# Kernel optimization log

Hardware: AMD Instinct MI355X
Metric: run time of the kernel (lower is better)

The kernel has to match this reference:

```python
import jax, jax.numpy as jnp
import numpy as np

EPS = 1e-7
CURVS = (1.0, 0.8, 1.2)
SCALES = (1.0, 0.8, 0.6)


def expmap0(v, c):
    sc = jnp.sqrt(c)
    n = jnp.maximum(jnp.linalg.norm(v, axis=-1, keepdims=True), EPS)
    return jnp.tanh(sc * n) * v / (sc * n)


def projx(x, c):
    max_n = (1.0 - 1e-5) / jnp.sqrt(c)
    n = jnp.maximum(jnp.linalg.norm(x, axis=-1, keepdims=True), EPS)
    return jnp.where(n > max_n, x * (max_n / n), x)


def logmap0(x, c):
    sc = jnp.sqrt(c)
    n = jnp.maximum(jnp.linalg.norm(x, axis=-1, keepdims=True), EPS)
    a = jnp.clip(sc * n, 0.0, 1.0 - 1e-7)
    return jnp.arctanh(a) * x / (sc * n)


def hamilton(q1, q2):
    # q1, q2: [..., 4] (w,x,y,z), broadcasting allowed
    w1, x1, y1, z1 = q1[..., 0], q1[..., 1], q1[..., 2], q1[..., 3]
    w2, x2, y2, z2 = q2[..., 0], q2[..., 1], q2[..., 2], q2[..., 3]
    w = w1 * w2 - x1 * x2 - y1 * y2 - z1 * z2
    x = w1 * x2 + x1 * w2 + y1 * z2 - z1 * y2
    y = w1 * y2 - x1 * z2 + y1 * w2 + z1 * x2
    z = w1 * z2 + x1 * y2 - y1 * x2 + z1 * w2
    return jnp.stack([w, x, y, z], axis=-1)


def mlp(v, Wa, ba, Wb, bb):
    # Linear -> GELU(exact, matching torch default) -> Linear; dropout is eval-mode identity
    return jax.nn.gelu(v @ Wa.T + ba, approximate=False) @ Wb.T + bb


def setup_inputs() -> dict:
    key = jax.random.key(0)
    ks = jax.random.split(key, 24)
    f32 = jnp.float32
    B = 65536
    d = {}
    d['x'] = jax.random.normal(ks[0], (B, 784), dtype=f32)
    # input embedding 784 -> 128, then to level-0 tangent space 128 -> 64
    d['W_in'] = jax.random.normal(ks[1], (128, 784), f32) * (1.0 / np.sqrt(784))
    d['b_in'] = jnp.zeros((128,), f32)
    d['W_tan'] = jax.random.normal(ks[2], (64, 128), f32) * (1.0 / np.sqrt(128))
    d['b_tan'] = jnp.zeros((64,), f32)
    # boundary-manifold tangent points per level (init_scale=0.01 as in BoundaryManifold)
    d['bp0'] = jax.random.normal(ks[3], (5, 64), f32) * 0.01
    d['bp1'] = jax.random.normal(ks[4], (3, 4), f32) * 0.01
    d['bp2'] = jax.random.normal(ks[5], (4, 32), f32) * 0.01
    # rotation 0->1: SO(64) via matrix exponential of a skew-symmetric generator
    d['A_rot'] = jax.random.normal(ks[6], (64, 64), f32) * 0.02
    # rotation 1->2: SO(4) via pvq unit quaternions (std=0.1 init as in source)
    d['p_quat'] = jax.random.normal(ks[7], (4,), f32) * 0.1
    d['q_quat'] = jax.random.normal(ks[8], (4,), f32) * 0.1
    # inter-level MLP transform 0->1: 64 -> 32 -> 4
    d['W0a'] = jax.random.normal(ks[9], (32, 64), f32) * (1.0 / np.sqrt(64))
    d['b0a'] = jnp.zeros((32,), f32)
    d['W0b'] = jax.random.normal(ks[10], (4, 32), f32) * (1.0 / np.sqrt(32))
    d['b0b'] = jnp.zeros((4,), f32)
    # inter-level MLP transform 1->2: 4 -> 16 -> 32
    d['W1a'] = jax.random.normal(ks[11], (16, 4), f32) * (1.0 / np.sqrt(4))
    d['b1a'] = jnp.zeros((16,), f32)
    d['W1b'] = jax.random.normal(ks[12], (32, 16), f32) * (1.0 / np.sqrt(16))
    d['b1b'] = jnp.zeros((32,), f32)
    # output head: concat_tangent (64+4+32=100) -> 10
    d['W_out'] = jax.random.normal(ks[13], (10, 100), f32) * (1.0 / np.sqrt(100))
    d['b_out'] = jnp.zeros((10,), f32)
    return d


def reference(x, W_in, b_in, W_tan, b_tan, bp0, bp1, bp2, A_rot, p_quat, q_quat,
              W0a, b0a, W0b, b0b, W1a, b1a, W1b, b1b, W_out, b_out):
    h = x @ W_in.T + b_in                       # [B, 128]
    v = h @ W_tan.T + b_tan                     # [B, 64] level-0 tangent vector
    bps = (bp0, bp1, bp2)
    level_tangents = []
    carried = None                              # boundary tangent vectors transformed from prev level
    for i in range(3):
        c, s = CURVS[i], SCALES[i]
        # scaled exp/log round trip through the Poincare ball of this level
        x_hyp = projx(expmap0(v * s, c), c)
        v_tan = logmap0(x_hyp, c) / s           # [B, d_i]
        # boundary manifold: tangent -> ball -> proj -> tangent
        b_own = logmap0(projx(expmap0(bps[i], c), c), c)  # [P_i, d_i]
        bnds = b_own if carried is None else jnp.concatenate([b_own, carried], axis=0)
        # relative vectors vs boundary points, mean-aggregated
        rel_agg = v_tan.mean(axis=0, keepdims=False) * 0 + (v_tan[:, None, :] - bnds[None, :, :]).mean(axis=1)  # [B, d_i]
        level_tangents.append(v_tan)
        v_comb = v_tan + rel_agg
        if i == 0:
            R = jax.scipy.linalg.expm(A_rot - A_rot.T)   # SO(64)
            v_rot = v_comb @ R.T
            b_rot = bnds @ R.T
            v = mlp(v_rot, W0a, b0a, W0b, b0b)
            carried = mlp(b_rot, W0a, b0a, W0b, b0b)
        elif i == 1:
            p = p_quat / (jnp.linalg.norm(p_quat) + EPS)
            q = q_quat / (jnp.linalg.norm(q_quat) + EPS)
            v_rot = hamilton(hamilton(p, v_comb), q)     # pvq SO(4) rotation
            b_rot = hamilton(hamilton(p, bnds), q)
            v = mlp(v_rot, W1a, b1a, W1b, b1b)
            carried = mlp(b_rot, W1a, b1a, W1b, b1b)
    agg = jnp.concatenate(level_tangents, axis=-1)       # [B, 100] concat_tangent
    return agg @ W_out.T + b_out                         # [B, 10]
```

## Files before the change

kernel.cpp:

```cpp
#include <hip/hip_runtime.h>
#include <hip/hip_bf16.h>

typedef __attribute__((ext_vector_type(4))) float f32x4;
typedef __attribute__((ext_vector_type(2))) unsigned int u32x2;
typedef __attribute__((ext_vector_type(4))) unsigned int u32x4;
typedef __attribute__((ext_vector_type(8))) short bf16x8;

#define EPSF 1e-7f

__device__ __forceinline__ float radial_factor(float sumsq, float c, float s){
  float sc = sqrtf(c);
  float nv = sqrtf(sumsq);
  float nu = fmaxf(s*nv, EPSF);
  float th = tanhf(sc*nu);
  float r1 = th/sc;
  float maxn = (1.0f - 1e-5f)/sc;
  float r2 = fminf(r1, maxn);
  float n1 = fmaxf(r2, EPSF);
  float a  = fminf(sc*n1, 1.0f - 1e-7f);
  float r3 = 0.5f*logf((1.0f + a)/(1.0f - a));
  return r3*r2/(sc*n1*nu);
}

__device__ __forceinline__ float gelu_f(float x){
  return 0.5f*x*(1.0f + erff(x*0.70710678118654752f));
}

__device__ __forceinline__ unsigned f2bf1(float f){
  unsigned u = __float_as_uint(f);
  return (u + 0x7FFFu + ((u>>16)&1u)) >> 16;
}
__device__ __forceinline__ unsigned f2bf_pk(float lo, float hi){
  unsigned ul = f2bf1(lo);
  unsigned uh = __float_as_uint(hi);
  uh = (uh + 0x7FFFu + ((uh>>16)&1u)) & 0xFFFF0000u;
  return ul | uh;
}

__device__ __forceinline__ void gload_lds16(const void* g, void* l){
  __builtin_amdgcn_global_load_lds((const __attribute__((address_space(1))) unsigned int*)g,
                                   (__attribute__((address_space(3))) unsigned int*)l,
                                   16, 0, 0);
}

#define WS_WC     0
#define WS_BCOMB  204800
#define WS_W0AE   205056
#define WS_BROT0  213248
#define WS_BOWN0  214528
#define WS_W0AT   215808
#define WS_MB0    224000
#define WS_MB1    224256
#define WS_W1AE   224272
#define WS_ZERO   224528
#define WS_V      225280

__global__ __launch_bounds__(256) void prep_a(
    const float* __restrict__ W_in, const float* __restrict__ b_in,
    const float* __restrict__ W_tan, const float* __restrict__ b_tan,
    const float* __restrict__ A_rot, const float* __restrict__ W0a,
    const float* __restrict__ bp0,
    unsigned short* __restrict__ Wc, float* __restrict__ bcomb,
    float* __restrict__ W0aE, float* __restrict__ brot0, float* __restrict__ bown0)
{
  __shared__ __align__(16) float Al[64][68];
  __shared__ __align__(16) float ST[64][68];
  const int bid = blockIdx.x, t = threadIdx.x;

  if (bid < 50){
    if (bid == 0 && t < 64){
      float s = b_tan[t];
      for (int j = 0; j < 128; ++j) s += b_in[j]*W_tan[t*128+j];
      bcomb[t] = s;
    }
    const int g4 = bid*256 + t;
    const int n = g4/200, k4 = (g4 - n*200)*4;
    f32x4 s = {0.f,0.f,0.f,0.f};
    if (k4 < 784){
      for (int j = 0; j < 128; ++j){
        float wt = W_tan[n*128+j];
        f32x4 wi = *(const f32x4*)(W_in + j*784 + k4);
        s += wt*wi;
      }
    }
    u32x2 st = { f2bf_pk(s[0], s[1]), f2bf_pk(s[2], s[3]) };
    const int tsl = k4 >> 5;
    const int q   = (k4 >> 3) & 3;
    const int qp  = q ^ ((n >> 1) & 3);
    const int idx = tsl*2048 + n*32 + qp*8 + (k4 & 7);
    *(u32x2*)(Wc + idx) = st;
  } else {
    for (int m = t; m < 4096; m += 256){
      int r = m >> 6, c = m & 63;
      Al[r][c] = A_rot[m];
    }
    __syncthreads();
    for (int m = t; m < 4096; m += 256){
      int r = m >> 6, c = m & 63;
      ST[r][c] = Al[c][r] - Al[r][c];
    }
    __syncthreads();
    const int wv = t >> 6, lane = t & 63;
    const int row = (bid - 50)*4 + wv;
    if (row < 37){
      float v, sgn;
      if (row < 32){ v = W0a[row*64 + lane]; sgn = 1.f; }
      else {
        const int r = row - 32;
        float b = bp0[r*64 + lane];
        float ssq = b*b;
        #pragma unroll
        for (int d = 1; d < 64; d <<= 1) ssq += __shfl_xor(ssq, d);
        float fc = radial_factor(ssq, 1.0f, 1.0f);
        v = b*fc;
        bown0[r*64 + lane] = v;
        sgn = -1.f;
      }
      float acc = v;
      for (int k = 1; k <= 12; ++k){
        const float coef = sgn/(float)k;
        float nv = 0.f;
        #pragma unroll
        for (int m = 0; m < 64; m += 4){
          f32x4 s4 = *(const f32x4*)&ST[lane][m];
          nv += __int_as_float(__builtin_amdgcn_readlane(__float_as_int(v), m+0))*s4[0];
          nv += __int_as_float(__builtin_amdgcn_readlane(__float_as_int(v), m+1))*s4[1];
          nv += __int_as_float(__builtin_amdgcn_readlane(__float_as_int(v), m+2))*s4[2];
          nv += __int_as_float(__builtin_amdgcn_readlane(__float_as_int(v), m+3))*s4[3];
        }
        nv *= coef;
        v = nv; acc += nv;
      }
      if (row < 32) W0aE[row*64 + lane] = acc;
      else          brot0[(row-32)*64 + lane] = acc;
    }
  }
}

__global__ __launch_bounds__(256) void prep_small(
    const float* __restrict__ bp1,
    const float* __restrict__ p_quat, const float* __restrict__ q_quat,
    const float* __restrict__ b0a, const float* __restrict__ W0b, const float* __restrict__ b0b,
    const float* __restrict__ W1a,
    const float* __restrict__ W0aE, const float* __restrict__ brot0, const float* __restrict__ bown0,
    float* __restrict__ W0aT, float* __restrict__ mb0, float* __restrict__ mb1,
    float* __restrict__ W1aE, float* __restrict__ zerog)
{
  __shared__ float g[5][32];
  __shared__ float c1[5][4];
  __shared__ float fac1[3];
  __shared__ float Mq[4][4];
  const int t = threadIdx.x;

  for (int i = t; i < 2048; i += 256){
    int o = i >> 6, k = i & 63;
    W0aT[k*32 + o] = W0aE[i];
  }
  if (t >= 240) zerog[t - 240] = 0.f;
  if (t < 64){
    float s = 0.f;
    for (int r = 0; r < 5; ++r) s += bown0[r*64 + t];
    mb0[t] = s * 0.2f;
  }
  if (t < 160){
    int r = t >> 5, o = t & 31;
    float s = b0a[o];
    for (int k = 0; k < 64; ++k) s += brot0[r*64+k]*W0aE[o*64+k];
    g[r][o] = gelu_f(s);
  }
  if (t >= 192 && t < 195){
    int r = t - 192;
    float ssq = 0.f;
    for (int j = 0; j < 4; ++j){ float b = bp1[r*4+j]; ssq += b*b; }
    fac1[r] = radial_factor(ssq, 0.8f, 1.0f);
  }
  if (t == 224){
    float pw=p_quat[0],px=p_quat[1],py=p_quat[2],pz=p_quat[3];
    float n1 = sqrtf(pw*pw+px*px+py*py+pz*pz) + EPSF;
    pw/=n1; px/=n1; py/=n1; pz/=n1;
    float qw=q_quat[0],qx=q_quat[1],qy=q_quat[2],qz=q_quat[3];
    float n2 = sqrtf(qw*qw+qx*qx+qy*qy+qz*qz) + EPSF;
    qw/=n2; qx/=n2; qy/=n2; qz/=n2;
    float Lp[4][4] = {{pw,-px,-py,-pz},{px,pw,-pz,py},{py,pz,pw,-px},{pz,-py,px,pw}};
    float Rq[4][4] = {{qw,-qx,-qy,-qz},{qx,qw,qz,-qy},{qy,-qz,qw,qx},{qz,qy,-qx,qw}};
    #pragma unroll
    for (int i = 0; i < 4; ++i)
      #pragma unroll
      for (int k = 0; k < 4; ++k){
        float s = 0.f;
        #pragma unroll
        for (int m = 0; m < 4; ++m) s += Rq[i][m]*Lp[m][k];
        Mq[i][k] = s;
      }
  }
  __syncthreads();
  if (t < 20){
    int r = t >> 2, o = t & 3;
    float s = b0b[o];
    for (int k = 0; k < 32; ++k) s += g[r][k]*W0b[o*32+k];
    c1[r][o] = s;
  }
  __syncthreads();
  if (t < 4){
    float s = 0.f;
    for (int r = 0; r < 3; ++r) s += bp1[r*4+t]*fac1[r];
    for (int r = 0; r < 5; ++r) s += c1[r][t];
    mb1[t] = s * 0.125f;
  }
  if (t >= 64 && t < 128){
    int i = t - 64, o = i >> 2, kq = i & 3;
    float s = 0.f;
    #pragma unroll
    for (int j = 0; j < 4; ++j) s += W1a[o*4+j]*Mq[j][kq];
    W1aE[o*4+kq] = s;
  }
}

__global__ __launch_bounds__(256, 6) void gemm_v(
    const float* __restrict__ x,
    const unsigned short* __restrict__ Wcs,
    const float* __restrict__ bcomb,
    const float* __restrict__ zerog,
    float* __restrict__ v)
{
  __shared__ __align__(16) char smem[24576];
  char* xsB  = smem;
  char* wcsB = smem + 16384;

  const int tid  = threadIdx.x;
  const int lane = tid & 63;
  const int w    = tid >> 6;
  const int wr   = w >> 1, wc = w & 1;
  const int lr   = lane & 15, lkg = lane >> 4;
  const size_t rowBase = (size_t)blockIdx.x * 64;

  const int row8 = lane >> 3;
  const int qs   = lane & 7;
  const int qoff = qs ^ row8;
  const float* xsrcA = x + (rowBase + (size_t)(8*w     + row8))*784 + qoff*4;
  const float* xsrcB = x + (rowBase + (size_t)(8*(w+4) + row8))*784 + qoff*4;
  const unsigned short* wsrc = Wcs + (16*w + (lane>>2))*32 + (lane&3)*8;

  const int rA0 = wr*32 + lr;
  const int sA0 = (2*lkg)     ^ (lr & 7);
  const int sA1 = (2*lkg + 1) ^ (lr & 7);
  const int offA00 = rA0*128 + sA0*16;
  const int offA01 = rA0*128 + sA1*16;
  const int rB0 = wc*32 + lr;
  const int sB  = lkg ^ ((rB0 >> 1) & 3);
  const int offB0 = rB0*64 + sB*16;

#define STAGE(slab, buf) do{                                                   \
    const int ks_ = (slab)*32;                                                 \
    char* xd_ = xsB  + (buf)*8192;                                             \
    char* wd_ = wcsB + (buf)*4096;                                             \
    const float* sa_ = (ks_ + qoff*4 < 784) ? (xsrcA + ks_) : zerog;           \
    const float* sb_ = (ks_ + qoff*4 < 784) ? (xsrcB + ks_) : zerog;           \
    gload_lds16(sa_, xd_ + w*1024);                                            \
    gload_lds16(sb_, xd_ + (w+4)*1024);                                        \
    gload_lds16(wsrc + (slab)*2048, wd_ + w*1024);                             \
  }while(0)

  STAGE(0, 0);
  __syncthreads();

  f32x4 acc00 = {}, acc01 = {}, acc10 = {}, acc11 = {};
  for (int t = 0; t < 25; ++t){
    const int cur = t & 1;
    if (t < 24) STAGE(t+1, cur^1);
    const char* xb = xsB  + cur*8192;
    const char* wb = wcsB + cur*4096;
    f32x4 a00 = *(const f32x4*)(xb + offA00);
    f32x4 a01 = *(const f32x4*)(xb + offA01);
    f32x4 a10 = *(const f32x4*)(xb + offA00 + 2048);
    f32x4 a11 = *(const f32x4*)(xb + offA01 + 2048);
    bf16x8 b0 = *(const bf16x8*)(wb + offB0);
    bf16x8 b1 = *(const bf16x8*)(wb + offB0 + 1024);
    u32x4 pk0 = { f2bf_pk(a00[0],a00[1]), f2bf_pk(a00[2],a00[3]),
                  f2bf_pk(a01[0],a01[1]), f2bf_pk(a01[2],a01[3]) };
    u32x4 pk1 = { f2bf_pk(a10[0],a10[1]), f2bf_pk(a10[2],a10[3]),
                  f2bf_pk(a11[0],a11[1]), f2bf_pk(a11[2],a11[3]) };
    bf16x8 af0 = __builtin_bit_cast(bf16x8, pk0);
    bf16x8 af1 = __builtin_bit_cast(bf16x8, pk1);
    acc00 = __builtin_amdgcn_mfma_f32_16x16x32_bf16(af0, b0, acc00, 0, 0, 0);
    acc01 = __builtin_amdgcn_mfma_f32_16x16x32_bf16(af0, b1, acc01, 0, 0, 0);
    acc10 = __builtin_amdgcn_mfma_f32_16x16x32_bf16(af1, b0, acc10, 0, 0, 0);
    acc11 = __builtin_amdgcn_mfma_f32_16x16x32_bf16(af1, b1, acc11, 0, 0, 0);
    __syncthreads();
  }
#undef STAGE

  {
    f32x4 accA[2][2] = { {acc00, acc01}, {acc10, acc11} };
    #pragma unroll
    for (int fj = 0; fj < 2; ++fj){
      const int col = wc*32 + fj*16 + lr;
      const float bc = bcomb[col];
      #pragma unroll
      for (int fi = 0; fi < 2; ++fi){
        const int r0 = wr*32 + fi*16 + lkg*4;
        #pragma unroll
        for (int j = 0; j < 4; ++j)
          v[(rowBase + (size_t)(r0 + j))*64 + col] = accA[fi][fj][j] + bc;
      }
    }
  }
}

__global__ __launch_bounds__(256, 4) void row_phase(
    const float* __restrict__ vg,
    const float* __restrict__ W0aT,
    const float* __restrict__ mb0g, const float* __restrict__ mb1g,
    const float* __restrict__ W1aEg,
    const float* __restrict__ b0a, const float* __restrict__ W0b, const float* __restrict__ b0b,
    const float* __restrict__ b1a, const float* __restrict__ W1b, const float* __restrict__ b1b,
    const float* __restrict__ Wout, const float* __restrict__ bout,
    float* __restrict__ out)
{
  __shared__ __align__(16) char smem[38304];
  float* vlds   = (float*)smem;
  float* gv     = (float*)(smem + 19456);
  float* cW0aTS = (float*)(smem + 28672);
  float* g1     = (float*)(smem + 28672);
  float* cW1bS  = (float*)(smem + 33792);
  float* cmb0S  = (float*)(smem + 36864);
  float* cW0bS  = (float*)(smem + 37120);
  float* cW1aES = (float*)(smem + 37632);
  float* cb0aS  = (float*)(smem + 37888);
  float* cb0bS  = (float*)(smem + 38016);
  float* cmb1S  = (float*)(smem + 38032);
  float* cb1aS  = (float*)(smem + 38048);
  float* cb1bS  = (float*)(smem + 38112);
  float* cboutS = (float*)(smem + 38240);

  const int tid = threadIdx.x;
  const size_t rowBase = (size_t)blockIdx.x * 64;

  for (int i = tid; i < 1024; i += 256){
    const int r = i >> 4, seg = i & 15;
    *(f32x4*)&vlds[r*76 + seg*4] = *(const f32x4*)(vg + (rowBase + (size_t)r)*64 + seg*4);
  }
  for (int i = tid; i < 2048; i += 256) cW0aTS[i] = W0aT[i];
  if (tid < 64)  cmb0S[tid] = mb0g[tid];
  if (tid < 32)  cb0aS[tid] = b0a[tid];
  if (tid < 128) cW0bS[tid] = W0b[tid];
  if (tid < 4)   { cb0bS[tid] = b0b[tid]; cmb1S[tid] = mb1g[tid]; }
  if (tid < 64)  cW1aES[tid] = W1aEg[tid];
  if (tid < 16)  cb1aS[tid] = b1a[tid];
  if (tid < 32)  cb1bS[tid] = b1b[tid];
  if (tid < 10)  cboutS[tid] = bout[tid];
  __syncthreads();

  const int row = tid >> 2, p4 = tid & 3;

  {
    f32x4 rv[4];
    float* vptr = &vlds[row*76 + p4*16];
    #pragma unroll
    for (int i = 0; i < 4; ++i) rv[i] = ((const f32x4*)vptr)[i];
    float ssq = 0.f;
    #pragma unroll
    for (int i = 0; i < 4; ++i)
      ssq += rv[i][0]*rv[i][0] + rv[i][1]*rv[i][1] + rv[i][2]*rv[i][2] + rv[i][3]*rv[i][3];
    ssq += __shfl_xor(ssq, 1); ssq += __shfl_xor(ssq, 2);
    const float fac = radial_factor(ssq, 1.0f, 1.0f);
    #pragma unroll
    for (int i = 0; i < 4; ++i){ rv[i] *= fac; ((f32x4*)vptr)[i] = rv[i]; }
  }
  __syncthreads();

  {
    const int og = p4;
    float a0o[8];
    #pragma unroll
    for (int j = 0; j < 8; ++j) a0o[j] = cb0aS[og*8 + j];
    #pragma unroll 4
    for (int k = 0; k < 64; k += 4){
      f32x4 vtv = *(const f32x4*)&vlds[row*76 + k];
      f32x4 mm  = *(const f32x4*)&cmb0S[k];
      #pragma unroll
      for (int u = 0; u < 4; ++u){
        const float vc = 2.f*vtv[u] - mm[u];
        const f32x4* wp = (const f32x4*)&cW0aTS[(k+u)*32 + og*8];
        f32x4 w0 = wp[0], w1 = wp[1];
        #pragma unroll
        for (int j = 0; j < 4; ++j){ a0o[j] += w0[j]*vc; a0o[4+j] += w1[j]*vc; }
      }
    }
    #pragma unroll
    for (int j = 0; j < 8; ++j) gv[row*36 + og*8 + j] = gelu_f(a0o[j]);
  }
  __syncthreads();

  {
    const int o1 = p4;
    float a1 = cb0bS[o1];
    #pragma unroll
    for (int k = 0; k < 32; k += 4){
      f32x4 gg = *(const f32x4*)&gv[row*36 + k];
      f32x4 ww = *(const f32x4*)&cW0bS[o1*32 + k];
      a1 += gg[0]*ww[0] + gg[1]*ww[1] + gg[2]*ww[2] + gg[3]*ww[3];
    }
    float ss1 = a1*a1;
    ss1 += __shfl_xor(ss1, 1); ss1 += __shfl_xor(ss1, 2);
    const float f1v = radial_factor(ss1, 0.8f, 0.8f);
    const float vt1 = a1*f1v;
    vlds[row*76 + 64 + o1] = vt1;
    vlds[row*76 + 68 + o1] = 2.f*vt1 - cmb1S[o1];
  }
  __syncthreads();

  for (int i = tid; i < 512; i += 256) cW1bS[i] = W1b[i];
  {
    const f32x4 vc1 = *(const f32x4*)&vlds[row*76 + 68];
    #pragma unroll
    for (int j = 0; j < 4; ++j){
      const int o = p4*4 + j;
      float s1 = cb1aS[o] + cW1aES[o*4+0]*vc1[0] + cW1aES[o*4+1]*vc1[1]
                          + cW1aES[o*4+2]*vc1[2] + cW1aES[o*4+3]*vc1[3];
      g1[row*20 + o] = gelu_f(s1);
    }
  }
  __syncthreads();

  {
    float v2[8]; float ss2 = 0.f;
    #pragma unroll
    for (int j = 0; j < 8; ++j){
      const int o = p4*8 + j;
      float s = cb1bS[o];
      #pragma unroll
      for (int k = 0; k < 16; k += 4){
        f32x4 gg = *(const f32x4*)&g1[row*20 + k];
        f32x4 ww = *(const f32x4*)&cW1bS[o*16 + k];
        s += gg[0]*ww[0] + gg[1]*ww[1] + gg[2]*ww[2] + gg[3]*ww[3];
      }
      v2[j] = s; ss2 += s*s;
    }
    ss2 += __shfl_xor(ss2, 1); ss2 += __shfl_xor(ss2, 2);
    const float f2v = radial_factor(ss2, 1.2f, 0.6f);
    #pragma unroll
    for (int j = 0; j < 8; ++j) gv[row*36 + p4*8 + j] = v2[j]*f2v;
  }
  __syncthreads();

  for (int idx = tid; idx < 640; idx += 256){
    const int r6 = idx/10, o = idx - r6*10;
    float s = cboutS[o];
    const float* wrow = Wout + o*100;
    const float* vrow = &vlds[r6*76];
    #pragma unroll 4
    for (int k = 0; k < 68; k += 4){
      f32x4 a = *(const f32x4*)(vrow + k);
      f32x4 b = *(const f32x4*)(wrow + k);
      s += a[0]*b[0] + a[1]*b[1] + a[2]*b[2] + a[3]*b[3];
    }
    const float* v2row = &gv[r6*36];
    #pragma unroll 4
    for (int k = 0; k < 32; k += 4){
      f32x4 a = *(const f32x4*)(v2row + k);
      f32x4 b = *(const f32x4*)(wrow + 68 + k);
      s += a[0]*b[0] + a[1]*b[1] + a[2]*b[2] + a[3]*b[3];
    }
    out[(rowBase + (size_t)r6)*10 + o] = s;
  }
}

extern "C" void kernel_launch(void* const* d_in, const int* in_sizes, int n_in,
                              void* d_out, int out_size, void* d_ws, size_t ws_size,
                              hipStream_t stream)
{
  (void)n_in; (void)out_size; (void)ws_size;
  const float* x      = (const float*)d_in[0];
  const float* W_in   = (const float*)d_in[1];
  const float* b_in   = (const float*)d_in[2];
  const float* W_tan  = (const float*)d_in[3];
  const float* b_tan  = (const float*)d_in[4];
  const float* bp0    = (const float*)d_in[5];
  const float* bp1    = (const float*)d_in[6];
  const float* A_rot  = (const float*)d_in[8];
  const float* p_quat = (const float*)d_in[9];
  const float* q_quat = (const float*)d_in[10];
  const float* W0a    = (const float*)d_in[11];
  const float* b0a    = (const float*)d_in[12];
  const float* W0b    = (const float*)d_in[13];
  const float* b0b    = (const float*)d_in[14];
  const float* W1a    = (const float*)d_in[15];
  const float* b1a    = (const float*)d_in[16];
  const float* W1b    = (const float*)d_in[17];
  const float* b1b    = (const float*)d_in[18];
  const float* W_out  = (const float*)d_in[19];
  const float* b_out  = (const float*)d_in[20];

  char* ws = (char*)d_ws;
  unsigned short* Wcs = (unsigned short*)(ws + WS_WC);
  float* bcomb = (float*)(ws + WS_BCOMB);
  float* W0aE  = (float*)(ws + WS_W0AE);
  float* brot0 = (float*)(ws + WS_BROT0);
  float* bown0 = (float*)(ws + WS_BOWN0);
  float* W0aT  = (float*)(ws + WS_W0AT);
  float* mb0   = (float*)(ws + WS_MB0);
  float* mb1   = (float*)(ws + WS_MB1);
  float* W1aE  = (float*)(ws + WS_W1AE);
  float* zerog = (float*)(ws + WS_ZERO);
  float* vbuf  = (float*)(ws + WS_V);

  const int Brows = in_sizes[0] / 784;
  const int nblk  = Brows / 64;

  prep_a<<<60, 256, 0, stream>>>(W_in, b_in, W_tan, b_tan, A_rot, W0a, bp0,
                                 Wcs, bcomb, W0aE, brot0, bown0);
  prep_small<<<1, 256, 0, stream>>>(bp1, p_quat, q_quat, b0a, W0b, b0b, W1a,
                                    W0aE, brot0, bown0, W0aT, mb0, mb1, W1aE, zerog);
  gemm_v<<<nblk, 256, 0, stream>>>(x, Wcs, bcomb, zerog, vbuf);
  row_phase<<<nblk, 256, 0, stream>>>(vbuf, W0aT, mb0, mb1, W1aE,
                                      b0a, W0b, b0b, b1a, W1b, b1b,
                                      W_out, b_out, (float*)d_out);
}
```

Measured before the change: 88.41 us.

## Triple-buffer gemm_v LDS staging with explicit vmcnt waits and barriers

Replaces the double-buffered loop in the input GEMM with a three-stage ring of LDS buffers. Each iteration waits with a partial s_waitcnt vmcnt so two slabs of global->LDS loads stay in flight, and a second barrier guards buffer reuse before the next prefetch is issued. LDS grows to 36 KB and launch bounds drop from 6 to 4 blocks per SM, giving deeper memory latency hiding at the cost of occupancy and an extra barrier per iteration.

```diff
diff --git a/kernel.cpp b/kernel.cpp
--- a/kernel.cpp
+++ b/kernel.cpp
@@ -216,16 +216,16 @@
   }
 }
 
-__global__ __launch_bounds__(256, 6) void gemm_v(
+__global__ __launch_bounds__(256, 4) void gemm_v(
     const float* __restrict__ x,
     const unsigned short* __restrict__ Wcs,
     const float* __restrict__ bcomb,
     const float* __restrict__ zerog,
     float* __restrict__ v)
 {
-  __shared__ __align__(16) char smem[24576];
+  __shared__ __align__(16) char smem[36864];
   char* xsB  = smem;
-  char* wcsB = smem + 16384;
+  char* wcsB = smem + 24576;
 
   const int tid  = threadIdx.x;
   const int lane = tid & 63;
@@ -258,36 +258,48 @@
     const float* sb_ = (ks_ + qoff*4 < 784) ? (xsrcB + ks_) : zerog;           \
     gload_lds16(sa_, xd_ + w*1024);                                            \
     gload_lds16(sb_, xd_ + (w+4)*1024);                                        \
-    gload_lds16(wsrc + (slab)*2048, wd_ + w*1024);                             \
+    gload_lds16(wsrc + (size_t)(slab)*2048, wd_ + w*1024);                     \
   }while(0)
 
-  STAGE(0, 0);
-  __syncthreads();
-
   f32x4 acc00 = {}, acc01 = {}, acc10 = {}, acc11 = {};
-  for (int t = 0; t < 25; ++t){
-    const int cur = t & 1;
-    if (t < 24) STAGE(t+1, cur^1);
-    const char* xb = xsB  + cur*8192;
-    const char* wb = wcsB + cur*4096;
-    f32x4 a00 = *(const f32x4*)(xb + offA00);
-    f32x4 a01 = *(const f32x4*)(xb + offA01);
-    f32x4 a10 = *(const f32x4*)(xb + offA00 + 2048);
-    f32x4 a11 = *(const f32x4*)(xb + offA01 + 2048);
-    bf16x8 b0 = *(const bf16x8*)(wb + offB0);
-    bf16x8 b1 = *(const bf16x8*)(wb + offB0 + 1024);
-    u32x4 pk0 = { f2bf_pk(a00[0],a00[1]), f2bf_pk(a00[2],a00[3]),
-                  f2bf_pk(a01[0],a01[1]), f2bf_pk(a01[2],a01[3]) };
-    u32x4 pk1 = { f2bf_pk(a10[0],a10[1]), f2bf_pk(a10[2],a10[3]),
-                  f2bf_pk(a11[0],a11[1]), f2bf_pk(a11[2],a11[3]) };
-    bf16x8 af0 = __builtin_bit_cast(bf16x8, pk0);
-    bf16x8 af1 = __builtin_bit_cast(bf16x8, pk1);
-    acc00 = __builtin_amdgcn_mfma_f32_16x16x32_bf16(af0, b0, acc00, 0, 0, 0);
-    acc01 = __builtin_amdgcn_mfma_f32_16x16x32_bf16(af0, b1, acc01, 0, 0, 0);
-    acc10 = __builtin_amdgcn_mfma_f32_16x16x32_bf16(af1, b0, acc10, 0, 0, 0);
-    acc11 = __builtin_amdgcn_mfma_f32_16x16x32_bf16(af1, b1, acc11, 0, 0, 0);
-    __syncthreads();
-  }
+
+#define BODY(tt, VMSTR) do{                                                    \
+    asm volatile("s_waitcnt " VMSTR ::: "memory");                             \
+    __builtin_amdgcn_sched_barrier(0);                                         \
+    __builtin_amdgcn_s_barrier();                                              \
+    const int cur_ = (tt) % 3;                                                 \
+    const char* xb_ = xsB  + cur_*8192;                                        \
+    const char* wb_ = wcsB + cur_*4096;                                        \
+    f32x4 a00_ = *(const f32x4*)(xb_ + offA00);                                \
+    f32x4 a01_ = *(const f32x4*)(xb_ + offA01);                                \
+    f32x4 a10_ = *(const f32x4*)(xb_ + offA00 + 2048);                         \
+    f32x4 a11_ = *(const f32x4*)(xb_ + offA01 + 2048);                         \
+    bf16x8 b0_ = *(const bf16x8*)(wb_ + offB0);                                \
+    bf16x8 b1_ = *(const bf16x8*)(wb_ + offB0 + 1024);                         \
+    u32x4 pk0_ = { f2bf_pk(a00_[0],a00_[1]), f2bf_pk(a00_[2],a00_[3]),         \
+                   f2bf_pk(a01_[0],a01_[1]), f2bf_pk(a01_[2],a01_[3]) };       \
+    u32x4 pk1_ = { f2bf_pk(a10_[0],a10_[1]), f2bf_pk(a10_[2],a10_[3]),         \
+                   f2bf_pk(a11_[0],a11_[1]), f2bf_pk(a11_[2],a11_[3]) };       \
+    bf16x8 af0_ = __builtin_bit_cast(bf16x8, pk0_);                            \
+    bf16x8 af1_ = __builtin_bit_cast(bf16x8, pk1_);                            \
+    acc00 = __builtin_amdgcn_mfma_f32_16x16x32_bf16(af0_, b0_, acc00, 0,0,0);  \
+    acc01 = __builtin_amdgcn_mfma_f32_16x16x32_bf16(af0_, b1_, acc01, 0,0,0);  \
+    acc10 = __builtin_amdgcn_mfma_f32_16x16x32_bf16(af1_, b0_, acc10, 0,0,0);  \
+    acc11 = __builtin_amdgcn_mfma_f32_16x16x32_bf16(af1_, b1_, acc11, 0,0,0);  \
+    asm volatile("s_waitcnt lgkmcnt(0)" ::: "memory");                         \
+    __builtin_amdgcn_sched_barrier(0);                                         \
+    __builtin_amdgcn_s_barrier();                                              \
+    if ((tt) + 3 < 25) STAGE((tt)+3, cur_);                                    \
+  }while(0)
+
+  STAGE(0, 0); STAGE(1, 1); STAGE(2, 2);
+
+  for (int t = 0; t < 23; ++t)
+    BODY(t, "vmcnt(6)");
+  BODY(23, "vmcnt(3)");
+  BODY(24, "vmcnt(0)");
+
+#undef BODY
 #undef STAGE
 
   {
```

New measurement: 88.35 us. About the same (-0.1%).
